# Kernel optimization log

Hardware: AMD Instinct MI355X
Metric: run time of the kernel (lower is better)

## Reference

```python
import jax, jax.numpy as jnp
import numpy as np

B, C, H, W = 8, 256, 64, 64
CQK = C // 8


def setup_inputs() -> dict:
    key = jax.random.key(0)
    ks = jax.random.split(key, 9)
    s_in = 1.0 / np.sqrt(C)
    return {
        "feature1": jax.random.normal(ks[0], (B, C, H, W), jnp.float32),
        "feature2": jax.random.normal(ks[1], (B, C, H, W), jnp.float32),
        "feature3": jax.random.normal(ks[2], (B, C, H, W), jnp.float32),
        # 1x1 conv weights stored as [out_ch, in_ch]
        "wq": jax.random.uniform(ks[3], (CQK, C), jnp.float32, -s_in, s_in),
        "bq": jax.random.uniform(ks[4], (CQK,), jnp.float32, -s_in, s_in),
        "wk": jax.random.uniform(ks[5], (CQK, C), jnp.float32, -s_in, s_in),
        "bk": jax.random.uniform(ks[6], (CQK,), jnp.float32, -s_in, s_in),
        "wv": jax.random.uniform(ks[7], (C, C), jnp.float32, -s_in, s_in),
        "bv": jax.random.uniform(ks[8], (C,), jnp.float32, -s_in, s_in),
    }


def reference(feature1, feature2, feature3, wq, bq, wk, bk, wv, bv):
    b, c, h, w = feature1.shape
    hw = h * w
    # 1x1 convs == per-pixel channel GEMMs
    q = jnp.einsum('bchw,oc->bohw', feature1, wq) + bq[None, :, None, None]
    k = jnp.einsum('bchw,oc->bohw', feature2, wk) + bk[None, :, None, None]
    v = jnp.einsum('bchw,oc->bohw', feature3, wv) + bv[None, :, None, None]
    q = q.reshape(b, -1, hw).transpose(0, 2, 1)  # [b, hw, cqk]
    k = k.reshape(b, -1, hw)                      # [b, cqk, hw]
    v = v.reshape(b, -1, hw)                      # [b, c, hw]
    attn = jax.nn.softmax(jnp.einsum('bnc,bcm->bnm', q, k), axis=-1)  # [b, hw, hw]
    # fused = value @ attn^T  -> [b, c, hw]
    fused = jnp.einsum('bcm,bnm->bcn', v, attn)
    return fused.reshape(b, c, h, w)
```

## Files before the change

### kernel.cpp

```cpp
#include <hip/hip_runtime.h>
#include <math.h>

#define BATCH 8
#define CH    256
#define HWPIX 4096
#define CQK_  32

typedef __bf16 bf16x8 __attribute__((ext_vector_type(8)));
typedef __bf16 bf16x4 __attribute__((ext_vector_type(4)));
typedef __bf16 bf16x2 __attribute__((ext_vector_type(2)));
typedef float  f32x4  __attribute__((ext_vector_type(4)));

#define FS_STR 68

static __device__ inline bf16x8 ld_frag(const __bf16* p) {
  bf16x4 lo = *(const bf16x4*)p;
  bf16x4 hi = *(const bf16x4*)(p + 4);
  return __builtin_shufflevector(lo, hi, 0, 1, 2, 3, 4, 5, 6, 7);
}

static __device__ inline bf16x8 w_frag(const float* p) {
  const float4 a = *(const float4*)p;
  const float4 b = *(const float4*)(p + 4);
  bf16x8 r;
  r[0] = (__bf16)a.x; r[1] = (__bf16)a.y; r[2] = (__bf16)a.z; r[3] = (__bf16)a.w;
  r[4] = (__bf16)b.x; r[5] = (__bf16)b.y; r[6] = (__bf16)b.z; r[7] = (__bf16)b.w;
  return r;
}

__global__ __launch_bounds__(512, 4) void proj_all(
    const float* __restrict__ f1, const float* __restrict__ f2,
    const float* __restrict__ f3,
    const float* __restrict__ wq, const float* __restrict__ bq,
    const float* __restrict__ wk, const float* __restrict__ bk,
    const float* __restrict__ wv, const float* __restrict__ bv,
    __bf16* __restrict__ qT, __bf16* __restrict__ kT, __bf16* __restrict__ vv)
{
  __shared__ __align__(16) __bf16 f_s[2][64 * FS_STR];
  const int t    = threadIdx.x;
  const int w    = __builtin_amdgcn_readfirstlane(t >> 6);
  const int lane = t & 63;
  const int q16  = lane & 15;
  const int quad = lane >> 4;
  const int b    = blockIdx.z;
  const int n0   = blockIdx.x * 64;
  const int mode = blockIdx.y;

  if (mode == 0) {
    const int half = t >> 8;
    const int th   = t & 255;
    const int sn   = (th & 15) * 4;
    const int scp  = (th >> 4) * 2;
    const int qr   = w & 3;
    const int isK  = w >> 2;

    const float* fsrc = (half ? f2 : f1) + (size_t)b * CH * HWPIX + n0;
    __bf16* fdst = f_s[half];

    f32x4 acc[2];
#pragma unroll
    for (int i = 0; i < 2; ++i) acc[i] = (f32x4){0.f, 0.f, 0.f, 0.f};

    float4 rg[4];
#pragma unroll
    for (int rr = 0; rr < 2; ++rr) {
      const int c = rr * 32 + scp;
      rg[2 * rr + 0] = *(const float4*)&fsrc[(size_t)(c)     * HWPIX + sn];
      rg[2 * rr + 1] = *(const float4*)&fsrc[(size_t)(c + 1) * HWPIX + sn];
    }

    const float* wmat = isK ? wk : wq;
    for (int c0 = 0; c0 < CH; c0 += 64) {
      __syncthreads();
#pragma unroll
      for (int rr = 0; rr < 2; ++rr) {
        const int c = rr * 32 + scp;
#pragma unroll
        for (int i = 0; i < 4; ++i) {
          bf16x2 pk;
          pk[0] = (__bf16)((const float*)&rg[2 * rr + 0])[i];
          pk[1] = (__bf16)((const float*)&rg[2 * rr + 1])[i];
          *(bf16x2*)&fdst[(sn + i) * FS_STR + c] = pk;
        }
      }
      __syncthreads();
      if (c0 < CH - 64) {
#pragma unroll
        for (int rr = 0; rr < 2; ++rr) {
          const int c = rr * 32 + scp;
          rg[2 * rr + 0] = *(const float4*)&fsrc[(size_t)(c0 + 64 + c)     * HWPIX + sn];
          rg[2 * rr + 1] = *(const float4*)&fsrc[(size_t)(c0 + 64 + c + 1) * HWPIX + sn];
        }
      }
      bf16x8 af[2];
#pragma unroll
      for (int kh = 0; kh < 2; ++kh)
        af[kh] = ld_frag(&f_s[isK][(16 * qr + q16) * FS_STR + 32 * kh + quad * 8]);
#pragma unroll
      for (int ot = 0; ot < 2; ++ot) {
#pragma unroll
        for (int kh = 0; kh < 2; ++kh) {
          const bf16x8 wf =
              w_frag(wmat + (size_t)(16 * ot + q16) * CH + c0 + 32 * kh + quad * 8);
          acc[ot] = __builtin_amdgcn_mfma_f32_16x16x32_bf16(af[kh], wf, acc[ot], 0, 0, 0);
        }
      }
    }
    const float* bias = isK ? bk : bq;
    __bf16* outT = isK ? kT : qT;
    const float b0 = bias[q16], b1 = bias[16 + q16];
#pragma unroll
    for (int r = 0; r < 4; ++r) {
      const size_t row = (size_t)b * HWPIX + n0 + 16 * qr + quad * 4 + r;
      outT[row * CQK_ + q16]      = (__bf16)(acc[0][r] + b0);
      outT[row * CQK_ + 16 + q16] = (__bf16)(acc[1][r] + b1);
    }
  } else {
    const int sn = (t & 15) * 4;
    const int c2 = (t >> 4) * 2;
    const float* f3b = f3 + (size_t)b * CH * HWPIX + n0;

    f32x4 acc[2][4];
#pragma unroll
    for (int ct = 0; ct < 2; ++ct)
#pragma unroll
      for (int nt = 0; nt < 4; ++nt) acc[ct][nt] = (f32x4){0.f, 0.f, 0.f, 0.f};

    float4 r0 = *(const float4*)&f3b[(size_t)(c2)     * HWPIX + sn];
    float4 r1 = *(const float4*)&f3b[(size_t)(c2 + 1) * HWPIX + sn];

    for (int c0 = 0; c0 < CH; c0 += 64) {
      __syncthreads();
#pragma unroll
      for (int i = 0; i < 4; ++i) {
        bf16x2 pk;
        pk[0] = (__bf16)((const float*)&r0)[i];
        pk[1] = (__bf16)((const float*)&r1)[i];
        *(bf16x2*)&f_s[0][(sn + i) * FS_STR + c2] = pk;
      }
      __syncthreads();
      if (c0 < CH - 64) {
        r0 = *(const float4*)&f3b[(size_t)(c0 + 64 + c2)     * HWPIX + sn];
        r1 = *(const float4*)&f3b[(size_t)(c0 + 64 + c2 + 1) * HWPIX + sn];
      }
      bf16x8 af[2][2];
#pragma unroll
      for (int ct = 0; ct < 2; ++ct)
#pragma unroll
        for (int kh = 0; kh < 2; ++kh)
          af[ct][kh] = w_frag(wv + (size_t)(32 * w + 16 * ct + q16) * CH
                              + c0 + 32 * kh + quad * 8);
#pragma unroll
      for (int nt = 0; nt < 4; ++nt) {
#pragma unroll
        for (int kh = 0; kh < 2; ++kh) {
          const bf16x8 bfr = ld_frag(&f_s[0][(16 * nt + q16) * FS_STR + 32 * kh + quad * 8]);
#pragma unroll
          for (int ct = 0; ct < 2; ++ct)
            acc[ct][nt] = __builtin_amdgcn_mfma_f32_16x16x32_bf16(
                af[ct][kh], bfr, acc[ct][nt], 0, 0, 0);
        }
      }
    }
#pragma unroll
    for (int ct = 0; ct < 2; ++ct) {
      const float4 bi = *(const float4*)&bv[32 * w + 16 * ct + quad * 4];
#pragma unroll
      for (int nt = 0; nt < 4; ++nt) {
#pragma unroll
        for (int r = 0; r < 4; ++r) {
          const int c = 32 * w + 16 * ct + quad * 4 + r;
          vv[((size_t)b * CH + c) * HWPIX + n0 + 16 * nt + q16] =
              (__bf16)(acc[ct][nt][r] + ((const float*)&bi)[r]);
        }
      }
    }
  }
}

__global__ __launch_bounds__(512, 4) void attn_kernel(
    const __bf16* __restrict__ qT, const __bf16* __restrict__ kT,
    const __bf16* __restrict__ vv, float* __restrict__ out)
{
  __shared__ __align__(16) __bf16 p_s[2][64 * 64];
  __shared__ float L_s[2][64];

  const int t    = threadIdx.x;
  const int w    = __builtin_amdgcn_readfirstlane(t >> 6);
  const int lane = t & 63;
  const int q16  = lane & 15;
  const int quad = lane >> 4;
  const int qb   = w & 3;
  const int hb   = w >> 2;
  const int swz  = (q16 & 7) << 4;

  const int b  = blockIdx.x & 7;
  const int q0 = (blockIdx.x >> 3) * 64;

  const __bf16* kTb = kT + (size_t)b * HWPIX * CQK_;
  const size_t koff = (size_t)(32 * hb + q16) * CQK_ + quad * 8;

  const __bf16* vp[2];
#pragma unroll
  for (int ct = 0; ct < 2; ++ct)
    vp[ct] = vv + ((size_t)b * CH + 32 * w + 16 * ct + q16) * HWPIX + quad * 8;

  const bf16x8 qfrag =
      *(const bf16x8*)(qT + ((size_t)b * HWPIX + q0 + 16 * qb + q16) * CQK_ + quad * 8);

  f32x4 oacc[2][4];
#pragma unroll
  for (int i = 0; i < 2; ++i)
#pragma unroll
    for (int j = 0; j < 4; ++j)
      oacc[i][j] = (f32x4){0.f, 0.f, 0.f, 0.f};
  float Lp = 0.f;

  bf16x8 kf[2];
#pragma unroll
  for (int mt = 0; mt < 2; ++mt)
    kf[mt] = *(const bf16x8*)(kTb + koff + mt * 512);
  {
    f32x4 Sv[2];
#pragma unroll
    for (int mt = 0; mt < 2; ++mt)
      Sv[mt] = __builtin_amdgcn_mfma_f32_16x16x32_bf16(
          kf[mt], qfrag, (f32x4){0.f, 0.f, 0.f, 0.f}, 0, 0, 0);
    const __bf16* kb1 = kTb + 64 * CQK_;
#pragma unroll
    for (int mt = 0; mt < 2; ++mt)
      kf[mt] = *(const bf16x8*)(kb1 + koff + mt * 512);
    char* pw = (char*)p_s[0] + (16 * qb + q16) * 128;
#pragma unroll
    for (int mt = 0; mt < 2; ++mt) {
      bf16x4 pk;
#pragma unroll
      for (int r = 0; r < 4; ++r) {
        const float e = __expf(Sv[mt][r]);
        Lp += e;
        pk[r] = (__bf16)e;
      }
      *(bf16x4*)(pw + ((64 * hb + 32 * mt + 8 * quad) ^ swz)) = pk;
    }
  }
  __syncthreads();

  for (int i = 0; i < 64; ++i) {
    bf16x8 vf[2][2];
#pragma unroll
    for (int ct = 0; ct < 2; ++ct)
#pragma unroll
      for (int mh = 0; mh < 2; ++mh)
        vf[ct][mh] = *(const bf16x8*)(vp[ct] + mh * 32);

    const char* pb = (const char*)p_s[i & 1];
    bf16x8 pf[4][2];
#pragma unroll
    for (int nt = 0; nt < 4; ++nt)
#pragma unroll
      for (int mh = 0; mh < 2; ++mh)
        pf[nt][mh] = *(const bf16x8*)(pb + (16 * nt + q16) * 128
                                      + ((64 * mh + 16 * quad) ^ swz));

    if (i < 63) {
      f32x4 Sv[2];
#pragma unroll
      for (int mt = 0; mt < 2; ++mt)
        Sv[mt] = __builtin_amdgcn_mfma_f32_16x16x32_bf16(
            kf[mt], qfrag, (f32x4){0.f, 0.f, 0.f, 0.f}, 0, 0, 0);
      const __bf16* kb2 = kTb + (size_t)((i + 2) & 63) * (64 * CQK_);
#pragma unroll
      for (int mt = 0; mt < 2; ++mt)
        kf[mt] = *(const bf16x8*)(kb2 + koff + mt * 512);
      char* pw = (char*)p_s[(i + 1) & 1] + (16 * qb + q16) * 128;
#pragma unroll
      for (int mt = 0; mt < 2; ++mt) {
        bf16x4 pk;
#pragma unroll
        for (int r = 0; r < 4; ++r) {
          const float e = __expf(Sv[mt][r]);
          Lp += e;
          pk[r] = (__bf16)e;
        }
        *(bf16x4*)(pw + ((64 * hb + 32 * mt + 8 * quad) ^ swz)) = pk;
      }
    }

#pragma unroll
    for (int ct = 0; ct < 2; ++ct)
#pragma unroll
      for (int nt = 0; nt < 4; ++nt)
#pragma unroll
        for (int mh = 0; mh < 2; ++mh)
          oacc[ct][nt] = __builtin_amdgcn_mfma_f32_16x16x32_bf16(
              vf[ct][mh], pf[nt][mh], oacc[ct][nt], 0, 0, 0);

#pragma unroll
    for (int ct = 0; ct < 2; ++ct) vp[ct] += 64;
    __syncthreads();
  }

  Lp += __shfl_xor(Lp, 16);
  Lp += __shfl_xor(Lp, 32);
  if (quad == 0) L_s[hb][16 * qb + q16] = Lp;
  __syncthreads();

  float rinv[4];
#pragma unroll
  for (int nt = 0; nt < 4; ++nt)
    rinv[nt] = 1.0f / (L_s[0][16 * nt + q16] + L_s[1][16 * nt + q16]);

  float* ob = out + ((size_t)b * CH + 32 * w) * HWPIX + q0;
#pragma unroll
  for (int ct = 0; ct < 2; ++ct)
#pragma unroll
    for (int r = 0; r < 4; ++r)
#pragma unroll
      for (int nt = 0; nt < 4; ++nt)
        ob[(size_t)(16 * ct + quad * 4 + r) * HWPIX + 16 * nt + q16] =
            oacc[ct][nt][r] * rinv[nt];
}

extern "C" void kernel_launch(void* const* d_in, const int* in_sizes, int n_in,
                              void* d_out, int out_size, void* d_ws, size_t ws_size,
                              hipStream_t stream)
{
  const float* f1 = (const float*)d_in[0];
  const float* f2 = (const float*)d_in[1];
  const float* f3 = (const float*)d_in[2];
  const float* wq = (const float*)d_in[3];
  const float* bq = (const float*)d_in[4];
  const float* wk = (const float*)d_in[5];
  const float* bk = (const float*)d_in[6];
  const float* wv = (const float*)d_in[7];
  const float* bv = (const float*)d_in[8];
  float* outp = (float*)d_out;

  __bf16* qTw = (__bf16*)d_ws;
  __bf16* kTw = qTw + (size_t)BATCH * HWPIX * CQK_;
  __bf16* vw  = kTw + (size_t)BATCH * HWPIX * CQK_;

  proj_all<<<dim3(64, 2, 8), 512, 0, stream>>>(f1, f2, f3, wq, bq, wk, bk, wv, bv,
                                               qTw, kTw, vw);
  attn_kernel<<<dim3(512), 512, 0, stream>>>(qTw, kTw, vw, outp);
}
```

Baseline: 305.4 us.

## Double key-tile size in attention loop and pixel tile in projection kernel

```diff
diff --git a/kernel.cpp b/kernel.cpp
--- a/kernel.cpp
+++ b/kernel.cpp
@@ -36,113 +36,122 @@
     const float* __restrict__ wv, const float* __restrict__ bv,
     __bf16* __restrict__ qT, __bf16* __restrict__ kT, __bf16* __restrict__ vv)
 {
-  __shared__ __align__(16) __bf16 f_s[2][64 * FS_STR];
+  __shared__ __align__(16) __bf16 f_s[2][128 * FS_STR];
   const int t    = threadIdx.x;
   const int w    = __builtin_amdgcn_readfirstlane(t >> 6);
   const int lane = t & 63;
   const int q16  = lane & 15;
   const int quad = lane >> 4;
   const int b    = blockIdx.z;
-  const int n0   = blockIdx.x * 64;
+  const int n0   = blockIdx.x * 128;
   const int mode = blockIdx.y;
 
   if (mode == 0) {
     const int half = t >> 8;
     const int th   = t & 255;
-    const int sn   = (th & 15) * 4;
-    const int scp  = (th >> 4) * 2;
+    const int px   = (th & 31) * 4;
+    const int g2   = (th >> 5) * 2;
+    const int isK  = w >> 2;
     const int qr   = w & 3;
-    const int isK  = w >> 2;
 
     const float* fsrc = (half ? f2 : f1) + (size_t)b * CH * HWPIX + n0;
     __bf16* fdst = f_s[half];
-
-    f32x4 acc[2];
-#pragma unroll
-    for (int i = 0; i < 2; ++i) acc[i] = (f32x4){0.f, 0.f, 0.f, 0.f};
-
-    float4 rg[4];
-#pragma unroll
-    for (int rr = 0; rr < 2; ++rr) {
-      const int c = rr * 32 + scp;
-      rg[2 * rr + 0] = *(const float4*)&fsrc[(size_t)(c)     * HWPIX + sn];
-      rg[2 * rr + 1] = *(const float4*)&fsrc[(size_t)(c + 1) * HWPIX + sn];
-    }
-
     const float* wmat = isK ? wk : wq;
+
+    f32x4 acc[2][2];
+#pragma unroll
+    for (int i = 0; i < 2; ++i)
+#pragma unroll
+      for (int j = 0; j < 2; ++j) acc[i][j] = (f32x4){0.f, 0.f, 0.f, 0.f};
+
+    float4 rg_[8];
+#define PLOAD(c0)                                                               \
+    _Pragma("unroll") for (int cc = 0; cc < 4; ++cc) {                          \
+      const int c = (c0) + 16 * cc + g2;                                        \
+      rg_[2 * cc]     = *(const float4*)&fsrc[(size_t)c * HWPIX + px];          \
+      rg_[2 * cc + 1] = *(const float4*)&fsrc[(size_t)(c + 1) * HWPIX + px];    \
+    }
+    PLOAD(0);
     for (int c0 = 0; c0 < CH; c0 += 64) {
       __syncthreads();
 #pragma unroll
-      for (int rr = 0; rr < 2; ++rr) {
-        const int c = rr * 32 + scp;
+      for (int cc = 0; cc < 4; ++cc) {
+        const int c = 16 * cc + g2;
 #pragma unroll
         for (int i = 0; i < 4; ++i) {
           bf16x2 pk;
-          pk[0] = (__bf16)((const float*)&rg[2 * rr + 0])[i];
-          pk[1] = (__bf16)((const float*)&rg[2 * rr + 1])[i];
-          *(bf16x2*)&fdst[(sn + i) * FS_STR + c] = pk;
+          pk[0] = (__bf16)((const float*)&rg_[2 * cc])[i];
+          pk[1] = (__bf16)((const float*)&rg_[2 * cc + 1])[i];
+          *(bf16x2*)&fdst[(px + i) * FS_STR + c] = pk;
         }
       }
       __syncthreads();
-      if (c0 < CH - 64) {
-#pragma unroll
-        for (int rr = 0; rr < 2; ++rr) {
-          const int c = rr * 32 + scp;
-          rg[2 * rr + 0] = *(const float4*)&fsrc[(size_t)(c0 + 64 + c)     * HWPIX + sn];
-          rg[2 * rr + 1] = *(const float4*)&fsrc[(size_t)(c0 + 64 + c + 1) * HWPIX + sn];
-        }
-      }
-      bf16x8 af[2];
-#pragma unroll
-      for (int kh = 0; kh < 2; ++kh)
-        af[kh] = ld_frag(&f_s[isK][(16 * qr + q16) * FS_STR + 32 * kh + quad * 8]);
-#pragma unroll
-      for (int ot = 0; ot < 2; ++ot) {
+      if (c0 < CH - 64) PLOAD(c0 + 64);
+      bf16x8 af[2][2];
+#pragma unroll
+      for (int rg = 0; rg < 2; ++rg)
+#pragma unroll
+        for (int kh = 0; kh < 2; ++kh)
+          af[rg][kh] = ld_frag(&f_s[isK][(32 * qr + 16 * rg + q16) * FS_STR
+                                         + 32 * kh + quad * 8]);
+#pragma unroll
+      for (int ot = 0; ot < 2; ++ot)
 #pragma unroll
         for (int kh = 0; kh < 2; ++kh) {
           const bf16x8 wf =
               w_frag(wmat + (size_t)(16 * ot + q16) * CH + c0 + 32 * kh + quad * 8);
-          acc[ot] = __builtin_amdgcn_mfma_f32_16x16x32_bf16(af[kh], wf, acc[ot], 0, 0, 0);
-        }
-      }
+#pragma unroll
+          for (int rg = 0; rg < 2; ++rg)
+            acc[ot][rg] = __builtin_amdgcn_mfma_f32_16x16x32_bf16(
+                af[rg][kh], wf, acc[ot][rg], 0, 0, 0);
+        }
     }
     const float* bias = isK ? bk : bq;
     __bf16* outT = isK ? kT : qT;
     const float b0 = bias[q16], b1 = bias[16 + q16];
 #pragma unroll
-    for (int r = 0; r < 4; ++r) {
-      const size_t row = (size_t)b * HWPIX + n0 + 16 * qr + quad * 4 + r;
-      outT[row * CQK_ + q16]      = (__bf16)(acc[0][r] + b0);
-      outT[row * CQK_ + 16 + q16] = (__bf16)(acc[1][r] + b1);
-    }
+    for (int rg = 0; rg < 2; ++rg)
+#pragma unroll
+      for (int r = 0; r < 4; ++r) {
+        const size_t row = (size_t)b * HWPIX + n0 + 32 * qr + 16 * rg + quad * 4 + r;
+        outT[row * CQK_ + q16]      = (__bf16)(acc[0][rg][r] + b0);
+        outT[row * CQK_ + 16 + q16] = (__bf16)(acc[1][rg][r] + b1);
+      }
+#undef PLOAD
   } else {
-    const int sn = (t & 15) * 4;
-    const int c2 = (t >> 4) * 2;
+    const int px = (t & 31) * 4;
+    const int g2 = (t >> 5) * 2;
     const float* f3b = f3 + (size_t)b * CH * HWPIX + n0;
 
-    f32x4 acc[2][4];
+    f32x4 acc[2][8];
 #pragma unroll
     for (int ct = 0; ct < 2; ++ct)
 #pragma unroll
-      for (int nt = 0; nt < 4; ++nt) acc[ct][nt] = (f32x4){0.f, 0.f, 0.f, 0.f};
-
-    float4 r0 = *(const float4*)&f3b[(size_t)(c2)     * HWPIX + sn];
-    float4 r1 = *(const float4*)&f3b[(size_t)(c2 + 1) * HWPIX + sn];
-
+      for (int nt = 0; nt < 8; ++nt) acc[ct][nt] = (f32x4){0.f, 0.f, 0.f, 0.f};
+
+    float4 r_[4];
+#define VLOAD(c0)                                                               \
+    _Pragma("unroll") for (int cc = 0; cc < 2; ++cc) {                          \
+      const int c = (c0) + 32 * cc + g2;                                        \
+      r_[2 * cc]     = *(const float4*)&f3b[(size_t)c * HWPIX + px];            \
+      r_[2 * cc + 1] = *(const float4*)&f3b[(size_t)(c + 1) * HWPIX + px];      \
+    }
+    VLOAD(0);
     for (int c0 = 0; c0 < CH; c0 += 64) {
       __syncthreads();
 #pragma unroll
-      for (int i = 0; i < 4; ++i) {
-        bf16x2 pk;
-        pk[0] = (__bf16)((const float*)&r0)[i];
-        pk[1] = (__bf16)((const float*)&r1)[i];
-        *(bf16x2*)&f_s[0][(sn + i) * FS_STR + c2] = pk;
+      for (int cc = 0; cc < 2; ++cc) {
+        const int c = 32 * cc + g2;
+#pragma unroll
+        for (int i = 0; i < 4; ++i) {
+          bf16x2 pk;
+          pk[0] = (__bf16)((const float*)&r_[2 * cc])[i];
+          pk[1] = (__bf16)((const float*)&r_[2 * cc + 1])[i];
+          *(bf16x2*)&f_s[0][(px + i) * FS_STR + c] = pk;
+        }
       }
       __syncthreads();
-      if (c0 < CH - 64) {
-        r0 = *(const float4*)&f3b[(size_t)(c0 + 64 + c2)     * HWPIX + sn];
-        r1 = *(const float4*)&f3b[(size_t)(c0 + 64 + c2 + 1) * HWPIX + sn];
-      }
+      if (c0 < CH - 64) VLOAD(c0 + 64);
       bf16x8 af[2][2];
 #pragma unroll
       for (int ct = 0; ct < 2; ++ct)
@@ -151,10 +160,11 @@
           af[ct][kh] = w_frag(wv + (size_t)(32 * w + 16 * ct + q16) * CH
                               + c0 + 32 * kh + quad * 8);
 #pragma unroll
-      for (int nt = 0; nt < 4; ++nt) {
+      for (int nt = 0; nt < 8; ++nt) {
 #pragma unroll
         for (int kh = 0; kh < 2; ++kh) {
-          const bf16x8 bfr = ld_frag(&f_s[0][(16 * nt + q16) * FS_STR + 32 * kh + quad * 8]);
+          const bf16x8 bfr =
+              ld_frag(&f_s[0][(16 * nt + q16) * FS_STR + 32 * kh + quad * 8]);
 #pragma unroll
           for (int ct = 0; ct < 2; ++ct)
             acc[ct][nt] = __builtin_amdgcn_mfma_f32_16x16x32_bf16(
@@ -166,7 +176,7 @@
     for (int ct = 0; ct < 2; ++ct) {
       const float4 bi = *(const float4*)&bv[32 * w + 16 * ct + quad * 4];
 #pragma unroll
-      for (int nt = 0; nt < 4; ++nt) {
+      for (int nt = 0; nt < 8; ++nt) {
 #pragma unroll
         for (int r = 0; r < 4; ++r) {
           const int c = 32 * w + 16 * ct + quad * 4 + r;
@@ -175,6 +185,7 @@
         }
       }
     }
+#undef VLOAD
   }
 }
 
@@ -182,7 +193,7 @@
     const __bf16* __restrict__ qT, const __bf16* __restrict__ kT,
     const __bf16* __restrict__ vv, float* __restrict__ out)
 {
-  __shared__ __align__(16) __bf16 p_s[2][64 * 64];
+  __shared__ __align__(16) __bf16 p_s[2][64 * 128];
   __shared__ float L_s[2][64];
 
   const int t    = threadIdx.x;
@@ -216,87 +227,86 @@
       oacc[i][j] = (f32x4){0.f, 0.f, 0.f, 0.f};
   float Lp = 0.f;
 
-  bf16x8 kf[2];
-#pragma unroll
-  for (int mt = 0; mt < 2; ++mt)
-    kf[mt] = *(const bf16x8*)(kTb + koff + mt * 512);
+  bf16x8 kf[4];
+#pragma unroll
+  for (int tm = 0; tm < 4; ++tm)
+    kf[tm] = *(const bf16x8*)(kTb + (size_t)(tm >> 1) * 2048 + (tm & 1) * 512 + koff);
   {
-    f32x4 Sv[2];
-#pragma unroll
-    for (int mt = 0; mt < 2; ++mt)
-      Sv[mt] = __builtin_amdgcn_mfma_f32_16x16x32_bf16(
-          kf[mt], qfrag, (f32x4){0.f, 0.f, 0.f, 0.f}, 0, 0, 0);
-    const __bf16* kb1 = kTb + 64 * CQK_;
-#pragma unroll
-    for (int mt = 0; mt < 2; ++mt)
-      kf[mt] = *(const bf16x8*)(kb1 + koff + mt * 512);
-    char* pw = (char*)p_s[0] + (16 * qb + q16) * 128;
-#pragma unroll
-    for (int mt = 0; mt < 2; ++mt) {
+    f32x4 Sv[4];
+#pragma unroll
+    for (int tm = 0; tm < 4; ++tm)
+      Sv[tm] = __builtin_amdgcn_mfma_f32_16x16x32_bf16(
+          kf[tm], qfrag, (f32x4){0.f, 0.f, 0.f, 0.f}, 0, 0, 0);
+    const __bf16* kb1 = kTb + 4096;
+#pragma unroll
+    for (int tm = 0; tm < 4; ++tm)
+      kf[tm] = *(const bf16x8*)(kb1 + (size_t)(tm >> 1) * 2048 + (tm & 1) * 512 + koff);
+    char* pw = (char*)p_s[0] + (16 * qb + q16) * 256;
+#pragma unroll
+    for (int tm = 0; tm < 4; ++tm) {
       bf16x4 pk;
 #pragma unroll
       for (int r = 0; r < 4; ++r) {
-        const float e = __expf(Sv[mt][r]);
+        const float e = __expf(Sv[tm][r]);
         Lp += e;
         pk[r] = (__bf16)e;
       }
-      *(bf16x4*)(pw + ((64 * hb + 32 * mt + 8 * quad) ^ swz)) = pk;
+      *(bf16x4*)(pw + ((128 * (tm >> 1) + 64 * hb + 32 * (tm & 1) + 8 * quad) ^ swz)) = pk;
     }
   }
   __syncthreads();
 
-  for (int i = 0; i < 64; ++i) {
-    bf16x8 vf[2][2];
+  for (int i = 0; i < 32; ++i) {
+    bf16x8 vf[2][4];
 #pragma unroll
     for (int ct = 0; ct < 2; ++ct)
 #pragma unroll
-      for (int mh = 0; mh < 2; ++mh)
+      for (int mh = 0; mh < 4; ++mh)
         vf[ct][mh] = *(const bf16x8*)(vp[ct] + mh * 32);
 
     const char* pb = (const char*)p_s[i & 1];
-    bf16x8 pf[4][2];
-#pragma unroll
-    for (int nt = 0; nt < 4; ++nt)
-#pragma unroll
-      for (int mh = 0; mh < 2; ++mh)
-        pf[nt][mh] = *(const bf16x8*)(pb + (16 * nt + q16) * 128
-                                      + ((64 * mh + 16 * quad) ^ swz));
-
-    if (i < 63) {
-      f32x4 Sv[2];
-#pragma unroll
-      for (int mt = 0; mt < 2; ++mt)
-        Sv[mt] = __builtin_amdgcn_mfma_f32_16x16x32_bf16(
-            kf[mt], qfrag, (f32x4){0.f, 0.f, 0.f, 0.f}, 0, 0, 0);
-      const __bf16* kb2 = kTb + (size_t)((i + 2) & 63) * (64 * CQK_);
-#pragma unroll
-      for (int mt = 0; mt < 2; ++mt)
-        kf[mt] = *(const bf16x8*)(kb2 + koff + mt * 512);
-      char* pw = (char*)p_s[(i + 1) & 1] + (16 * qb + q16) * 128;
-#pragma unroll
-      for (int mt = 0; mt < 2; ++mt) {
+
+    if (i < 31) {
+      f32x4 Sv[4];
+#pragma unroll
+      for (int tm = 0; tm < 4; ++tm)
+        Sv[tm] = __builtin_amdgcn_mfma_f32_16x16x32_bf16(
+            kf[tm], qfrag, (f32x4){0.f, 0.f, 0.f, 0.f}, 0, 0, 0);
+      const __bf16* kb2 = kTb + (size_t)((i + 2) & 31) * 4096;
+#pragma unroll
+      for (int tm = 0; tm < 4; ++tm)
+        kf[tm] = *(const bf16x8*)(kb2 + (size_t)(tm >> 1) * 2048 + (tm & 1) * 512 + koff);
+      char* pw = (char*)p_s[(i + 1) & 1] + (16 * qb + q16) * 256;
+#pragma unroll
+      for (int tm = 0; tm < 4; ++tm) {
         bf16x4 pk;
 #pragma unroll
         for (int r = 0; r < 4; ++r) {
-          const float e = __expf(Sv[mt][r]);
+          const float e = __expf(Sv[tm][r]);
           Lp += e;
           pk[r] = (__bf16)e;
         }
-        *(bf16x4*)(pw + ((64 * hb + 32 * mt + 8 * quad) ^ swz)) = pk;
-      }
-    }
-
-#pragma unroll
-    for (int ct = 0; ct < 2; ++ct)
+        *(bf16x4*)(pw + ((128 * (tm >> 1) + 64 * hb + 32 * (tm & 1) + 8 * quad) ^ swz)) = pk;
+      }
+    }
+
+#pragma unroll
+    for (int mh = 0; mh < 4; ++mh) {
+      bf16x8 pf[4];
 #pragma unroll
       for (int nt = 0; nt < 4; ++nt)
-#pragma unroll
-        for (int mh = 0; mh < 2; ++mh)
+        pf[nt] = *(const bf16x8*)(pb + (16 * nt + q16) * 256
+                                  + ((64 * mh + 16 * quad) ^ swz));
+#pragma unroll
+      for (int ct = 0; ct < 2; ++ct)
+#pragma unroll
+        for (int nt = 0; nt < 4; ++nt)
           oacc[ct][nt] = __builtin_amdgcn_mfma_f32_16x16x32_bf16(
-              vf[ct][mh], pf[nt][mh], oacc[ct][nt], 0, 0, 0);
-
-#pragma unroll
-    for (int ct = 0; ct < 2; ++ct) vp[ct] += 64;
+              vf[ct][mh], pf[nt], oacc[ct][nt], 0, 0, 0);
+    }
+
+#pragma unroll
+    for (int ct = 0; ct < 2; ++ct) vp[ct] += 128;
     __syncthreads();
   }
 
@@ -340,7 +350,7 @@
   __bf16* kTw = qTw + (size_t)BATCH * HWPIX * CQK_;
   __bf16* vw  = kTw + (size_t)BATCH * HWPIX * CQK_;
 
-  proj_all<<<dim3(64, 2, 8), 512, 0, stream>>>(f1, f2, f3, wq, bq, wk, bk, wv, bv,
+  proj_all<<<dim3(32, 2, 8), 512, 0, stream>>>(f1, f2, f3, wq, bq, wk, bk, wv, bv,
                                                qTw, kTw, vw);
   attn_kernel<<<dim3(512), 512, 0, stream>>>(qTw, kTw, vw, outp);
 }
```

After: 295.6 us. 1.03x faster.
